# Kernel optimization log

Measured on AMD Instinct MI355X. Metric: run time of the kernel, lower is better.

## Reference

```python
import jax, jax.numpy as jnp
import numpy as np
from jax import lax

B, C, H, W, S = 8, 64, 64, 64, 12
KSIZE = 5


def _conv2d_same(x, w):
    # x: [N, Cin, H, W], w: [Cout, Cin, kh, kw]
    return lax.conv_general_dilated(
        x, w, window_strides=(1, 1), padding='SAME',
        dimension_numbers=('NCHW', 'OIHW', 'NCHW'))


def setup_inputs() -> dict:
    key = jax.random.key(0)
    k0, k1, k2, k3, k4 = jax.random.split(key, 5)
    x = jax.random.normal(k0, (B, C, H, W, S), dtype=jnp.float32)
    w1 = jax.random.normal(k1, (3 * C, C, 1, 1), dtype=jnp.float32) * 0.05
    b1 = jax.random.normal(k2, (3 * C,), dtype=jnp.float32) * 0.05
    w2 = jax.random.normal(k3, (1, 2 * C, KSIZE, KSIZE), dtype=jnp.float32) * 0.05
    b2 = jax.random.normal(k4, (1,), dtype=jnp.float32) * 0.05
    return {'x': x, 'w1': w1, 'b1': b1, 'w2': w2, 'b2': b2}


def reference(x, w1, b1, w2, b2):
    b, c, h, w_, s = x.shape
    # conv1 (1x1) applied per timestep == channel matmul over all timesteps at once
    qkv = jnp.einsum('oc,bchws->bohws', w1[:, :, 0, 0], x) + b1[None, :, None, None, None]
    Q, K, V = jnp.split(qkv, 3, axis=1)  # each [b, c, h, w, s]

    # conv2 on concat(Q_s, K_t) is linear in channels:
    # score(s,t) = convQ(Q[...,s]) + convK(K[...,t]) + bias
    def per_time_conv(z, wsub):
        # z: [b, c, h, w, s] -> fold time into batch -> conv -> [b, h, w, s]
        zb = jnp.moveaxis(z, -1, 1).reshape(b * s, c, h, w_)
        out = _conv2d_same(zb, wsub)  # [b*s, 1, h, w]
        return jnp.moveaxis(out.reshape(b, s, h, w_), 1, -1)  # [b, h, w, s]

    A_q = per_time_conv(Q, w2[:, :c])   # [b, h, w, s] (query index)
    A_k = per_time_conv(K, w2[:, c:])   # [b, h, w, t] (key index)

    # scores: [b, h, w, t, s]
    scores = A_q[:, :, :, None, :] + A_k[:, :, :, :, None] + b2[0]
    attn = jax.nn.softmax(scores, axis=-2)  # softmax over t (keys)

    # weighted sum of V over t -> [b, c, h, w, s]
    V_out = jnp.einsum('bhwts,bchwt->bchws', attn, V)
    return V_out
```

## Files before the change

kernel.cpp:

```cpp
#include <hip/hip_runtime.h>
#include <hip/hip_bf16.h>

#define X_B 8
#define X_C 64
#define X_H 64
#define X_W 64
#define X_S 12

#define WEFF_OFF 0
#define PART_OFF 4096
#define PART_SZ  393216

__global__ __launch_bounds__(256) void k_prep(const float* __restrict__ w1,
                                              const float* __restrict__ w2,
                                              float* __restrict__ weff) {
    int idx = blockIdx.x * 256 + threadIdx.x;
    if (idx >= 64 * 25) return;
    int cp = idx / 25, tap = idx % 25;
    float s = 0.f;
    for (int c = 0; c < 64; ++c)
        s = fmaf(w2[(64 + c) * 25 + tap], w1[(64 + c) * 64 + cp], s);
    weff[cp * 25 + tap] = s;
}

__global__ __launch_bounds__(128) void k_conv(const float* __restrict__ x,
                                              const float* __restrict__ weff,
                                              float* __restrict__ part) {
    const int bid   = blockIdx.x;
    const int b     = bid & 7;
    const int strip = (bid >> 3) & 3;
    const int tg    = (bid >> 5) % 3;
    const int q     = bid / 96;

    const int w   = threadIdx.x & 63;
    const int hq  = threadIdx.x >> 6;
    const int htb = strip * 16 + hq * 8;

    float acc[8][4];
#pragma unroll
    for (int o = 0; o < 8; ++o)
#pragma unroll
        for (int j = 0; j < 4; ++j) acc[o][j] = 0.f;

    for (int ci = 0; ci < 4; ++ci) {
        const int c = q * 4 + ci;
        const float* wp = weff + c * 25;
        float wgt[25];
#pragma unroll
        for (int k = 0; k < 25; ++k) wgt[k] = wp[k];

        const float* xc = x + (size_t)(b * 64 + c) * 49152 + tg * 4;
#pragma unroll
        for (int rr = 0; rr < 12; ++rr) {
            const int r = htb - 2 + rr;
            if (r < 0 || r >= 64) continue;
            const float* xr = xc + r * 768;
#pragma unroll
            for (int dw = 0; dw < 5; ++dw) {
                const int wc = w + dw - 2;
                const bool ok = ((unsigned)wc < 64u);
                const int wcc = ok ? wc : 0;
                float4 v = *(const float4*)(xr + wcc * 12);
                if (!ok) { v.x = 0.f; v.y = 0.f; v.z = 0.f; v.w = 0.f; }
                const int olo = (rr - 4 < 0) ? 0 : rr - 4;
                const int ohi = (rr > 7) ? 7 : rr;
#pragma unroll
                for (int o = olo; o <= ohi; ++o) {
                    const float g = wgt[(rr - o) * 5 + dw];
                    acc[o][0] = fmaf(g, v.x, acc[o][0]);
                    acc[o][1] = fmaf(g, v.y, acc[o][1]);
                    acc[o][2] = fmaf(g, v.z, acc[o][2]);
                    acc[o][3] = fmaf(g, v.w, acc[o][3]);
                }
            }
        }
    }

    float* pb = part + (size_t)q * PART_SZ;
#pragma unroll
    for (int o = 0; o < 8; ++o) {
        const int h = htb + o;
        float4 st; st.x = acc[o][0]; st.y = acc[o][1]; st.z = acc[o][2]; st.w = acc[o][3];
        *(float4*)(pb + (size_t)((b * 64 + h) * 64 + w) * 12 + tg * 4) = st;
    }
}

__global__ __launch_bounds__(256) void k_soft(const float* __restrict__ part,
                                              float* __restrict__ p) {
    const int idx = blockIdx.x * 256 + threadIdx.x;
    if (idx >= 32768) return;
    float v[12];
#pragma unroll
    for (int t = 0; t < 12; ++t) v[t] = 0.f;
#pragma unroll
    for (int qg = 0; qg < 16; ++qg) {
        const float* pp = part + (size_t)qg * PART_SZ + (size_t)idx * 12;
        float4 t0 = *(const float4*)(pp);
        float4 t1 = *(const float4*)(pp + 4);
        float4 t2 = *(const float4*)(pp + 8);
        v[0] += t0.x; v[1] += t0.y; v[2]  += t0.z; v[3]  += t0.w;
        v[4] += t1.x; v[5] += t1.y; v[6]  += t1.z; v[7]  += t1.w;
        v[8] += t2.x; v[9] += t2.y; v[10] += t2.z; v[11] += t2.w;
    }
    float m = v[0];
#pragma unroll
    for (int t = 1; t < 12; ++t) m = fmaxf(m, v[t]);
    float s = 0.f;
#pragma unroll
    for (int t = 0; t < 12; ++t) { v[t] = __expf(v[t] - m); s += v[t]; }
    const float inv = 1.f / s;
#pragma unroll
    for (int t = 0; t < 12; ++t) v[t] *= inv;
    float* op = p + (size_t)idx * 12;
    float4 s0; s0.x = v[0]; s0.y = v[1]; s0.z = v[2];  s0.w = v[3];
    float4 s1; s1.x = v[4]; s1.y = v[5]; s1.z = v[6];  s1.w = v[7];
    float4 s2; s2.x = v[8]; s2.y = v[9]; s2.z = v[10]; s2.w = v[11];
    *(float4*)(op)     = s0;
    *(float4*)(op + 4) = s1;
    *(float4*)(op + 8) = s2;
}

__global__ __launch_bounds__(512) void k_out(const float* __restrict__ x,
                                             const float* __restrict__ w1,
                                             const float* __restrict__ b1,
                                             const float* __restrict__ p,
                                             float* __restrict__ out) {
    __shared__ float lds[64 * 65];

    const int b  = blockIdx.x >> 6;
    const int h  = blockIdx.x & 63;
    const int w  = threadIdx.x & 63;
    const int cg = threadIdx.x >> 6;

    const float* pp = p + (size_t)((b * 64 + h) * 64 + w) * 12;
    float pv[12];
    {
        float4 t0 = *(const float4*)(pp);
        float4 t1 = *(const float4*)(pp + 4);
        float4 t2 = *(const float4*)(pp + 8);
        pv[0] = t0.x; pv[1] = t0.y; pv[2]  = t0.z; pv[3]  = t0.w;
        pv[4] = t1.x; pv[5] = t1.y; pv[6]  = t1.z; pv[7]  = t1.w;
        pv[8] = t2.x; pv[9] = t2.y; pv[10] = t2.z; pv[11] = t2.w;
    }

    const float* xb0 = x + ((size_t)(b * 64 + cg * 8) * 64 + h) * 768 + w * 12;
#pragma unroll
    for (int j = 0; j < 8; ++j) {
        const float* xp = xb0 + (size_t)j * 49152;
        float4 u0 = *(const float4*)(xp);
        float4 u1 = *(const float4*)(xp + 4);
        float4 u2 = *(const float4*)(xp + 8);
        float s = 0.f;
        s = fmaf(pv[0], u0.x, s);  s = fmaf(pv[1], u0.y, s);
        s = fmaf(pv[2], u0.z, s);  s = fmaf(pv[3], u0.w, s);
        s = fmaf(pv[4], u1.x, s);  s = fmaf(pv[5], u1.y, s);
        s = fmaf(pv[6], u1.z, s);  s = fmaf(pv[7], u1.w, s);
        s = fmaf(pv[8], u2.x, s);  s = fmaf(pv[9], u2.y, s);
        s = fmaf(pv[10], u2.z, s); s = fmaf(pv[11], u2.w, s);
        lds[w * 65 + cg * 8 + j] = s;
    }
    __syncthreads();

    const float* w1v = w1 + 128 * 64 + cg * 8 * 64;
    float acc[8];
#pragma unroll
    for (int j = 0; j < 8; ++j) acc[j] = b1[128 + cg * 8 + j];
    for (int c2 = 0; c2 < 64; ++c2) {
        const float xv = lds[w * 65 + c2];
#pragma unroll
        for (int j = 0; j < 8; ++j)
            acc[j] = fmaf(w1v[j * 64 + c2], xv, acc[j]);
    }

#pragma unroll
    for (int j = 0; j < 8; ++j) {
        const int co = cg * 8 + j;
        float4 f; f.x = acc[j]; f.y = acc[j]; f.z = acc[j]; f.w = acc[j];
        float* op = out + ((size_t)(b * 64 + co) * 4096 + h * 64 + w) * 12;
        *(float4*)(op)     = f;
        *(float4*)(op + 4) = f;
        *(float4*)(op + 8) = f;
    }
}

extern "C" void kernel_launch(void* const* d_in, const int* in_sizes, int n_in,
                              void* d_out, int out_size, void* d_ws, size_t ws_size,
                              hipStream_t stream) {
    const float* x  = (const float*)d_in[0];
    const float* w1 = (const float*)d_in[1];
    const float* b1 = (const float*)d_in[2];
    const float* w2 = (const float*)d_in[3];

    float* outp = (float*)d_out;
    float* weff = outp + WEFF_OFF;
    float* part = outp + PART_OFF;
    float* p    = (float*)d_ws;

    hipLaunchKernelGGL(k_prep, dim3(7),    dim3(256), 0, stream, w1, w2, weff);
    hipLaunchKernelGGL(k_conv, dim3(1536), dim3(128), 0, stream, x, weff, part);
    hipLaunchKernelGGL(k_soft, dim3(128),  dim3(256), 0, stream, part, p);
    hipLaunchKernelGGL(k_out,  dim3(512),  dim3(512), 0, stream, x, w1, b1, p, outp);
}
```

Measured before the change: 99.62 us.

## Stage conv input tiles in LDS with register prefetch and tg-planar partials

Measured after the change: 104.0 us. 1.04x slower.

```diff
diff --git a/kernel.cpp b/kernel.cpp
--- a/kernel.cpp
+++ b/kernel.cpp
@@ -10,6 +10,7 @@
 #define WEFF_OFF 0
 #define PART_OFF 4096
 #define PART_SZ  393216
+#define TG_SZ    131072
 
 __global__ __launch_bounds__(256) void k_prep(const float* __restrict__ w1,
                                               const float* __restrict__ w2,
@@ -23,65 +24,120 @@
     weff[cp * 25 + tap] = s;
 }
 
-__global__ __launch_bounds__(128) void k_conv(const float* __restrict__ x,
+#define PLANE 5444
+#define ROWP  272
+__global__ __launch_bounds__(256) void k_conv(const float* __restrict__ x,
                                               const float* __restrict__ weff,
                                               float* __restrict__ part) {
+    __shared__ float lds[3 * PLANE];
+
     const int bid   = blockIdx.x;
     const int b     = bid & 7;
     const int strip = (bid >> 3) & 3;
-    const int tg    = (bid >> 5) % 3;
-    const int q     = bid / 96;
-
-    const int w   = threadIdx.x & 63;
-    const int hq  = threadIdx.x >> 6;
-    const int htb = strip * 16 + hq * 8;
-
-    float acc[8][4];
-#pragma unroll
-    for (int o = 0; o < 8; ++o)
-#pragma unroll
-        for (int j = 0; j < 4; ++j) acc[o][j] = 0.f;
+    const int q     = bid >> 5;
+
+    const int w  = threadIdx.x & 63;
+    const int hq = threadIdx.x >> 6;
+    const int r0 = strip * 16 - 2;
+
+    if (threadIdx.x < 240) {
+        const int pl  = threadIdx.x / 80;
+        const int rem = threadIdx.x % 80;
+        const int row = rem >> 2;
+        const int sl  = rem & 3;
+        const int slot = (sl < 2) ? sl : 64 + sl;
+        float4 z; z.x = 0.f; z.y = 0.f; z.z = 0.f; z.w = 0.f;
+        *(float4*)(lds + pl * PLANE + row * ROWP + slot * 4) = z;
+    }
+
+    const float* xb = x + (size_t)(b * 64 + q * 4) * 49152;
+
+    float acc[4][12];
+#pragma unroll
+    for (int o = 0; o < 4; ++o)
+#pragma unroll
+        for (int j = 0; j < 12; ++j) acc[o][j] = 0.f;
+
+    float4 pf[15];
+#pragma unroll
+    for (int k = 0; k < 15; ++k) {
+        const int rrr = k / 3, it = k % 3;
+        const int r  = hq + rrr * 4;
+        const int rg = r0 + r;
+        const int j  = it * 64 + w;
+        float4 v; v.x = 0.f; v.y = 0.f; v.z = 0.f; v.w = 0.f;
+        if ((unsigned)rg < 64u) v = *(const float4*)(xb + rg * 768 + j * 4);
+        pf[k] = v;
+    }
 
     for (int ci = 0; ci < 4; ++ci) {
-        const int c = q * 4 + ci;
-        const float* wp = weff + c * 25;
+#pragma unroll
+        for (int k = 0; k < 15; ++k) {
+            const int rrr = k / 3, it = k % 3;
+            const int r = hq + rrr * 4;
+            const unsigned j = (unsigned)(it * 64 + w);
+            const unsigned wj = j / 3u;
+            const unsigned tg = j - wj * 3u;
+            *(float4*)(lds + tg * PLANE + r * ROWP + (wj + 2) * 4) = pf[k];
+        }
+        __syncthreads();
+
+        if (ci < 3) {
+            const float* xc = xb + (size_t)(ci + 1) * 49152;
+#pragma unroll
+            for (int k = 0; k < 15; ++k) {
+                const int rrr = k / 3, it = k % 3;
+                const int r  = hq + rrr * 4;
+                const int rg = r0 + r;
+                const int j  = it * 64 + w;
+                float4 v; v.x = 0.f; v.y = 0.f; v.z = 0.f; v.w = 0.f;
+                if ((unsigned)rg < 64u) v = *(const float4*)(xc + rg * 768 + j * 4);
+                pf[k] = v;
+            }
+        }
+
+        const float* wp = weff + (q * 4 + ci) * 25;
         float wgt[25];
 #pragma unroll
         for (int k = 0; k < 25; ++k) wgt[k] = wp[k];
 
-        const float* xc = x + (size_t)(b * 64 + c) * 49152 + tg * 4;
-#pragma unroll
-        for (int rr = 0; rr < 12; ++rr) {
-            const int r = htb - 2 + rr;
-            if (r < 0 || r >= 64) continue;
-            const float* xr = xc + r * 768;
-#pragma unroll
-            for (int dw = 0; dw < 5; ++dw) {
-                const int wc = w + dw - 2;
-                const bool ok = ((unsigned)wc < 64u);
-                const int wcc = ok ? wc : 0;
-                float4 v = *(const float4*)(xr + wcc * 12);
-                if (!ok) { v.x = 0.f; v.y = 0.f; v.z = 0.f; v.w = 0.f; }
-                const int olo = (rr - 4 < 0) ? 0 : rr - 4;
-                const int ohi = (rr > 7) ? 7 : rr;
-#pragma unroll
-                for (int o = olo; o <= ohi; ++o) {
-                    const float g = wgt[(rr - o) * 5 + dw];
-                    acc[o][0] = fmaf(g, v.x, acc[o][0]);
-                    acc[o][1] = fmaf(g, v.y, acc[o][1]);
-                    acc[o][2] = fmaf(g, v.z, acc[o][2]);
-                    acc[o][3] = fmaf(g, v.w, acc[o][3]);
+#pragma unroll
+        for (int tg = 0; tg < 3; ++tg) {
+            const float* lr0 = lds + tg * PLANE + (hq * 4) * ROWP + w * 4;
+#pragma unroll
+            for (int rr = 0; rr < 8; ++rr) {
+                const float* lp = lr0 + rr * ROWP;
+#pragma unroll
+                for (int dw = 0; dw < 5; ++dw) {
+                    float4 v = *(const float4*)(lp + dw * 4);
+                    const int olo = (rr - 4 < 0) ? 0 : rr - 4;
+                    const int ohi = (rr > 3) ? 3 : rr;
+#pragma unroll
+                    for (int oo = olo; oo <= ohi; ++oo) {
+                        const float g = wgt[(rr - oo) * 5 + dw];
+                        acc[oo][tg * 4 + 0] = fmaf(g, v.x, acc[oo][tg * 4 + 0]);
+                        acc[oo][tg * 4 + 1] = fmaf(g, v.y, acc[oo][tg * 4 + 1]);
+                        acc[oo][tg * 4 + 2] = fmaf(g, v.z, acc[oo][tg * 4 + 2]);
+                        acc[oo][tg * 4 + 3] = fmaf(g, v.w, acc[oo][tg * 4 + 3]);
+                    }
                 }
             }
         }
+        __syncthreads();
     }
 
     float* pb = part + (size_t)q * PART_SZ;
 #pragma unroll
-    for (int o = 0; o < 8; ++o) {
-        const int h = htb + o;
-        float4 st; st.x = acc[o][0]; st.y = acc[o][1]; st.z = acc[o][2]; st.w = acc[o][3];
-        *(float4*)(pb + (size_t)((b * 64 + h) * 64 + w) * 12 + tg * 4) = st;
+    for (int oo = 0; oo < 4; ++oo) {
+        const int h = strip * 16 + hq * 4 + oo;
+        const int idx = (b * 64 + h) * 64 + w;
+#pragma unroll
+        for (int tg = 0; tg < 3; ++tg) {
+            float4 st;
+            st.x = acc[oo][tg * 4 + 0]; st.y = acc[oo][tg * 4 + 1];
+            st.z = acc[oo][tg * 4 + 2]; st.w = acc[oo][tg * 4 + 3];
+            *(float4*)(pb + (size_t)tg * TG_SZ + (size_t)idx * 4) = st;
+        }
     }
 }
 
@@ -94,13 +150,13 @@
     for (int t = 0; t < 12; ++t) v[t] = 0.f;
 #pragma unroll
     for (int qg = 0; qg < 16; ++qg) {
-        const float* pp = part + (size_t)qg * PART_SZ + (size_t)idx * 12;
-        float4 t0 = *(const float4*)(pp);
-        float4 t1 = *(const float4*)(pp + 4);
-        float4 t2 = *(const float4*)(pp + 8);
-        v[0] += t0.x; v[1] += t0.y; v[2]  += t0.z; v[3]  += t0.w;
-        v[4] += t1.x; v[5] += t1.y; v[6]  += t1.z; v[7]  += t1.w;
-        v[8] += t2.x; v[9] += t2.y; v[10] += t2.z; v[11] += t2.w;
+        const float* pp = part + (size_t)qg * PART_SZ;
+#pragma unroll
+        for (int tg = 0; tg < 3; ++tg) {
+            float4 t0 = *(const float4*)(pp + (size_t)tg * TG_SZ + (size_t)idx * 4);
+            v[tg * 4 + 0] += t0.x; v[tg * 4 + 1] += t0.y;
+            v[tg * 4 + 2] += t0.z; v[tg * 4 + 3] += t0.w;
+        }
     }
     float m = v[0];
 #pragma unroll
@@ -197,7 +253,7 @@
     float* p    = (float*)d_ws;
 
     hipLaunchKernelGGL(k_prep, dim3(7),    dim3(256), 0, stream, w1, w2, weff);
-    hipLaunchKernelGGL(k_conv, dim3(1536), dim3(128), 0, stream, x, weff, part);
+    hipLaunchKernelGGL(k_conv, dim3(512),  dim3(256), 0, stream, x, weff, part);
     hipLaunchKernelGGL(k_soft, dim3(128),  dim3(256), 0, stream, part, p);
     hipLaunchKernelGGL(k_out,  dim3(512),  dim3(512), 0, stream, x, w1, b1, p, outp);
 }
```

## Restructure 5x5 conv as per-pixel tap projections followed by a shifted gather-sum

Applied to the files above, without the earlier changes.

Result: slower. 118.0 us (+18.5%).

```diff
diff --git a/kernel.cpp b/kernel.cpp
--- a/kernel.cpp
+++ b/kernel.cpp
@@ -1,15 +1,9 @@
 #include <hip/hip_runtime.h>
 #include <hip/hip_bf16.h>
 
-#define X_B 8
-#define X_C 64
-#define X_H 64
-#define X_W 64
-#define X_S 12
-
 #define WEFF_OFF 0
-#define PART_OFF 4096
-#define PART_SZ  393216
+#define Y_OFF    4096
+#define Y_PLANE  393216
 
 __global__ __launch_bounds__(256) void k_prep(const float* __restrict__ w1,
                                               const float* __restrict__ w2,
@@ -23,95 +17,85 @@
     weff[cp * 25 + tap] = s;
 }
 
-__global__ __launch_bounds__(128) void k_conv(const float* __restrict__ x,
-                                              const float* __restrict__ weff,
-                                              float* __restrict__ part) {
-    const int bid   = blockIdx.x;
-    const int b     = bid & 7;
-    const int strip = (bid >> 3) & 3;
-    const int tg    = (bid >> 5) % 3;
-    const int q     = bid / 96;
+__global__ __launch_bounds__(128) void k_tap(const float* __restrict__ x,
+                                             const float* __restrict__ weff,
+                                             float* __restrict__ y) {
+    const int n  = blockIdx.x * 128 + threadIdx.x;
+    const int m  = n / 3;
+    const int tg = n - m * 3;
+    const int w  = m & 63;
+    const int h  = (m >> 6) & 63;
+    const int b  = m >> 12;
 
-    const int w   = threadIdx.x & 63;
-    const int hq  = threadIdx.x >> 6;
-    const int htb = strip * 16 + hq * 8;
+    const float* xp = x + (size_t)b * 3145728 + h * 768 + w * 12 + tg * 4;
 
-    float acc[8][4];
+    float4 acc[25];
 #pragma unroll
-    for (int o = 0; o < 8; ++o)
+    for (int k = 0; k < 25; ++k) { acc[k].x = 0.f; acc[k].y = 0.f; acc[k].z = 0.f; acc[k].w = 0.f; }
+
+    float4 v = *(const float4*)(xp);
+    for (int c = 0; c < 64; ++c) {
+        float4 vn;
+        if (c < 63) vn = *(const float4*)(xp + (c + 1) * 49152);
+        const float* wg = weff + c * 25;
 #pragma unroll
-        for (int j = 0; j < 4; ++j) acc[o][j] = 0.f;
+        for (int k = 0; k < 25; ++k) {
+            const float g = wg[k];
+            acc[k].x = fmaf(g, v.x, acc[k].x);
+            acc[k].y = fmaf(g, v.y, acc[k].y);
+            acc[k].z = fmaf(g, v.z, acc[k].z);
+            acc[k].w = fmaf(g, v.w, acc[k].w);
+        }
+        v = vn;
+    }
 
-    for (int ci = 0; ci < 4; ++ci) {
-        const int c = q * 4 + ci;
-        const float* wp = weff + c * 25;
-        float wgt[25];
 #pragma unroll
-        for (int k = 0; k < 25; ++k) wgt[k] = wp[k];
+    for (int k = 0; k < 25; ++k)
+        *(float4*)(y + (size_t)k * Y_PLANE + (size_t)n * 4) = acc[k];
+}
 
-        const float* xc = x + (size_t)(b * 64 + c) * 49152 + tg * 4;
+__global__ __launch_bounds__(64) void k_gather(const float* __restrict__ y,
+                                               float* __restrict__ p) {
+    const int m = blockIdx.x * 64 + threadIdx.x;
+    const int w = m & 63;
+    const int h = (m >> 6) & 63;
+    const int b = m >> 12;
+
+    float v[12];
 #pragma unroll
-        for (int rr = 0; rr < 12; ++rr) {
-            const int r = htb - 2 + rr;
-            if (r < 0 || r >= 64) continue;
-            const float* xr = xc + r * 768;
+    for (int t = 0; t < 12; ++t) v[t] = 0.f;
+
 #pragma unroll
-            for (int dw = 0; dw < 5; ++dw) {
-                const int wc = w + dw - 2;
-                const bool ok = ((unsigned)wc < 64u);
-                const int wcc = ok ? wc : 0;
-                float4 v = *(const float4*)(xr + wcc * 12);
-                if (!ok) { v.x = 0.f; v.y = 0.f; v.z = 0.f; v.w = 0.f; }
-                const int olo = (rr - 4 < 0) ? 0 : rr - 4;
-                const int ohi = (rr > 7) ? 7 : rr;
+    for (int dh = 0; dh < 5; ++dh) {
+        const int hh = h + dh - 2;
+        if ((unsigned)hh >= 64u) continue;
+        const int rowm = (b * 64 + hh) * 64;
 #pragma unroll
-                for (int o = olo; o <= ohi; ++o) {
-                    const float g = wgt[(rr - o) * 5 + dw];
-                    acc[o][0] = fmaf(g, v.x, acc[o][0]);
-                    acc[o][1] = fmaf(g, v.y, acc[o][1]);
-                    acc[o][2] = fmaf(g, v.z, acc[o][2]);
-                    acc[o][3] = fmaf(g, v.w, acc[o][3]);
-                }
-            }
+        for (int dw = 0; dw < 5; ++dw) {
+            const int ww = w + dw - 2;
+            if ((unsigned)ww >= 64u) continue;
+            const float* yp = y + (size_t)(dh * 5 + dw) * Y_PLANE
+                                + (size_t)(rowm + ww) * 12;
+            float4 a0 = *(const float4*)(yp);
+            float4 a1 = *(const float4*)(yp + 4);
+            float4 a2 = *(const float4*)(yp + 8);
+            v[0] += a0.x; v[1] += a0.y; v[2]  += a0.z; v[3]  += a0.w;
+            v[4] += a1.x; v[5] += a1.y; v[6]  += a1.z; v[7]  += a1.w;
+            v[8] += a2.x; v[9] += a2.y; v[10] += a2.z; v[11] += a2.w;
         }
     }
 
-    float* pb = part + (size_t)q * PART_SZ;
+    float mx = v[0];
 #pragma unroll
-    for (int o = 0; o < 8; ++o) {
-        const int h = htb + o;
-        float4 st; st.x = acc[o][0]; st.y = acc[o][1]; st.z = acc[o][2]; st.w = acc[o][3];
-        *(float4*)(pb + (size_t)((b * 64 + h) * 64 + w) * 12 + tg * 4) = st;
-    }
-}
-
-__global__ __launch_bounds__(256) void k_soft(const float* __restrict__ part,
-                                              float* __restrict__ p) {
-    const int idx = blockIdx.x * 256 + threadIdx.x;
-    if (idx >= 32768) return;
-    float v[12];
-#pragma unroll
-    for (int t = 0; t < 12; ++t) v[t] = 0.f;
-#pragma unroll
-    for (int qg = 0; qg < 16; ++qg) {
-        const float* pp = part + (size_t)qg * PART_SZ + (size_t)idx * 12;
-        float4 t0 = *(const float4*)(pp);
-        float4 t1 = *(const float4*)(pp + 4);
-        float4 t2 = *(const float4*)(pp + 8);
-        v[0] += t0.x; v[1] += t0.y; v[2]  += t0.z; v[3]  += t0.w;
-        v[4] += t1.x; v[5] += t1.y; v[6]  += t1.z; v[7]  += t1.w;
-        v[8] += t2.x; v[9] += t2.y; v[10] += t2.z; v[11] += t2.w;
-    }
-    float m = v[0];
-#pragma unroll
-    for (int t = 1; t < 12; ++t) m = fmaxf(m, v[t]);
+    for (int t = 1; t < 12; ++t) mx = fmaxf(mx, v[t]);
     float s = 0.f;
 #pragma unroll
-    for (int t = 0; t < 12; ++t) { v[t] = __expf(v[t] - m); s += v[t]; }
+    for (int t = 0; t < 12; ++t) { v[t] = __expf(v[t] - mx); s += v[t]; }
     const float inv = 1.f / s;
 #pragma unroll
     for (int t = 0; t < 12; ++t) v[t] *= inv;
-    float* op = p + (size_t)idx * 12;
+
+    float* op = p + (size_t)m * 12;
     float4 s0; s0.x = v[0]; s0.y = v[1]; s0.z = v[2];  s0.w = v[3];
     float4 s1; s1.x = v[4]; s1.y = v[5]; s1.z = v[6];  s1.w = v[7];
     float4 s2; s2.x = v[8]; s2.y = v[9]; s2.z = v[10]; s2.w = v[11];
@@ -193,11 +177,11 @@
 
     float* outp = (float*)d_out;
     float* weff = outp + WEFF_OFF;
-    float* part = outp + PART_OFF;
+    float* y    = outp + Y_OFF;
     float* p    = (float*)d_ws;
 
-    hipLaunchKernelGGL(k_prep, dim3(7),    dim3(256), 0, stream, w1, w2, weff);
-    hipLaunchKernelGGL(k_conv, dim3(1536), dim3(128), 0, stream, x, weff, part);
-    hipLaunchKernelGGL(k_soft, dim3(128),  dim3(256), 0, stream, part, p);
-    hipLaunchKernelGGL(k_out,  dim3(512),  dim3(512), 0, stream, x, w1, b1, p, outp);
+    hipLaunchKernelGGL(k_prep,   dim3(7),    dim3(256), 0, stream, w1, w2, weff);
+    hipLaunchKernelGGL(k_tap,    dim3(768),  dim3(128), 0, stream, x, weff, y);
+    hipLaunchKernelGGL(k_gather, dim3(512),  dim3(64),  0, stream, y, p);
+    hipLaunchKernelGGL(k_out,    dim3(512),  dim3(512), 0, stream, x, w1, b1, p, outp);
 }
```
